# Kernel tuning notes

Hardware: AMD Instinct MI355X
Metric: run time of the kernel (lower is better)

Reference implementation:

```python
import jax, jax.numpy as jnp
from jax import lax
import numpy as np

T, B, H, NUM_DATA, IN_DIM = 2048, 256, 128, 4096, 1


def setup_inputs() -> dict:
    key = jax.random.key(0)
    ks = jax.random.split(key, 9)
    s = 1.0 / np.sqrt(H)  # PyTorch LSTM/Linear default init scale
    inp = {
        "input": jax.random.normal(ks[0], (T, B, IN_DIM), dtype=jnp.float32),
        "label": jax.random.randint(ks[1], (B,), 0, NUM_DATA),
        "h0": jnp.zeros((1, NUM_DATA, H), dtype=jnp.float32),
        "W_ih": jax.random.uniform(ks[2], (4 * H, IN_DIM), jnp.float32, -s, s),
        "W_hh": jax.random.uniform(ks[3], (4 * H, H), jnp.float32, -s, s),
        "b_ih": jax.random.uniform(ks[4], (4 * H,), jnp.float32, -s, s),
        "b_hh": jax.random.uniform(ks[5], (4 * H,), jnp.float32, -s, s),
        "W_lin": jax.random.uniform(ks[6], (IN_DIM, H), jnp.float32, -s, s),
        "b_lin": jax.random.uniform(ks[7], (IN_DIM,), jnp.float32, -s, s),
    }
    return inp


def reference(input, label, h0, W_ih, W_hh, b_ih, b_hh, W_lin, b_lin):
    seq_len = input.shape[0]
    num_in_batch = input.shape[1]
    # Gather learned initial hidden state per sequence id (the python cat loop in torch)
    h = h0[0, label]                                   # (B, H)
    c = jnp.zeros_like(h)                              # (B, H)
    y0 = jnp.zeros((num_in_batch, IN_DIM), input.dtype)  # t=0 input is zeros
    b = b_ih + b_hh                                    # (4H,)

    def step(carry, _):
        h, c, x = carry
        gates = x @ W_ih.T + h @ W_hh.T + b            # (B, 4H); torch gate order i,f,g,o
        i, f, g, o = jnp.split(gates, 4, axis=-1)
        i = jax.nn.sigmoid(i)
        f = jax.nn.sigmoid(f)
        g = jnp.tanh(g)
        o = jax.nn.sigmoid(o)
        c = f * c + i * g
        h = o * jnp.tanh(c)
        y = h @ W_lin.T + b_lin                        # (B, 1) -> fed back as next input
        return (h, c, y), y

    _, ys = lax.scan(step, (h, c, y0), None, length=seq_len)
    return ys  # (T, B, 1), matches torch cat of (1, B, 1) along dim 0
```

## Files before the change

### kernel.cpp

```cpp
#include <hip/hip_runtime.h>
#include <math.h>

#define T_STEPS 2048
#define BATCH   256
#define HDIM    128

__device__ __forceinline__ float fast_rcp(float x) { return __builtin_amdgcn_rcpf(x); }
__device__ __forceinline__ float sigmoid_f(float x) { return fast_rcp(1.0f + __expf(-x)); }
__device__ __forceinline__ float tanh_f(float x) {
    float e = __expf(2.0f * x);
    return 1.0f - 2.0f * fast_rcp(e + 1.0f);
}

#define REP8(M) M(0) M(1) M(2) M(3) M(4) M(5) M(6) M(7)

__global__ __launch_bounds__(512, 2)
void lstm_seq_kernel(const int*   __restrict__ label,
                     const float* __restrict__ h0,
                     const float* __restrict__ W_ih,
                     const float* __restrict__ W_hh,
                     const float* __restrict__ b_ih,
                     const float* __restrict__ b_hh,
                     const float* __restrict__ W_lin,
                     const float* __restrict__ b_lin,
                     float*       __restrict__ out)
{
    const int tid   = threadIdx.x;
    const int batch = blockIdx.x;
    const int m     = tid >> 2;
    const int q     = tid & 3;
    const int q8    = q * 8;

    const int ri = m, rf = m + 128, rg = m + 256, ro = m + 384;

    __shared__ __attribute__((aligned(16))) float hist[128 * 144];

    const float4* W4 = (const float4*)W_hh;
    const float4* L4 = (const float4*)W_lin;

    #define DECL_W(i) \
        float4 wi##i = W4[ri * 32 + q8 + (i)]; \
        float4 wf##i = W4[rf * 32 + q8 + (i)]; \
        float4 wg##i = W4[rg * 32 + q8 + (i)]; \
        float4 wo##i = W4[ro * 32 + q8 + (i)];
    REP8(DECL_W)

    const float wih_i = W_ih[ri], wih_f = W_ih[rf];
    const float wih_g = W_ih[rg], wih_o = W_ih[ro];
    const float blin  = b_lin[0];

    const float bi_ = b_ih[ri] + b_hh[ri] + wih_i * blin;
    const float bf_ = b_ih[rf] + b_hh[rf] + wih_f * blin;
    const float bg_ = b_ih[rg] + b_hh[rg] + wih_g * blin;
    const float bo_ = b_ih[ro] + b_hh[ro] + wih_o * blin;

    const float SNEG = -0x1.715476p+0f;
    const float SG   =  0x1.715476p+1f;
    const float bi4s = bi_ * 0.25f * SNEG;
    const float bf4s = bf_ * 0.25f * SNEG;
    const float bg4s = bg_ * 0.25f * SG;
    const float bo4s = bo_ * 0.25f * SNEG;

    #define FOLD_W(i) { float4 lv = L4[q8 + (i)]; \
        wi##i.x = fmaf(wih_i, lv.x, wi##i.x); wi##i.y = fmaf(wih_i, lv.y, wi##i.y); \
        wi##i.z = fmaf(wih_i, lv.z, wi##i.z); wi##i.w = fmaf(wih_i, lv.w, wi##i.w); \
        wf##i.x = fmaf(wih_f, lv.x, wf##i.x); wf##i.y = fmaf(wih_f, lv.y, wf##i.y); \
        wf##i.z = fmaf(wih_f, lv.z, wf##i.z); wf##i.w = fmaf(wih_f, lv.w, wf##i.w); \
        wg##i.x = fmaf(wih_g, lv.x, wg##i.x); wg##i.y = fmaf(wih_g, lv.y, wg##i.y); \
        wg##i.z = fmaf(wih_g, lv.z, wg##i.z); wg##i.w = fmaf(wih_g, lv.w, wg##i.w); \
        wo##i.x = fmaf(wih_o, lv.x, wo##i.x); wo##i.y = fmaf(wih_o, lv.y, wo##i.y); \
        wo##i.z = fmaf(wih_o, lv.z, wo##i.z); wo##i.w = fmaf(wih_o, lv.w, wo##i.w); }
    REP8(FOLD_W)

    const int   lane = tid & 63;
    const int   ya0w = lane + ((lane >> 5) << 2);
    const float wl_a = W_lin[lane];
    const float wl_b = W_lin[lane + 64];
    const int   hword = m + ((m >> 5) << 2);

    float* slotI = &hist[144 * 127];
    if (tid < HDIM) slotI[tid + ((tid >> 5) << 2)] = h0[label[batch] * HDIM + tid];
    __syncthreads();

    float p0 = slotI[ya0w] * wl_a + slotI[ya0w + 72] * wl_b;
    #pragma unroll
    for (int off = 1; off < 64; off <<= 1) p0 += __shfl_xor(p0, off, 64);
    const float y0 = p0 + blin;

    const float cbi = bi_ - wih_i * y0;
    const float cbf = bf_ - wih_f * y0;
    const float cbg = bg_ - wih_g * y0;
    const float cbo = bo_ - wih_o * y0;

    const float4* hq0 = (const float4*)(slotI + 36 * q);
    float ai = 0.f, af = 0.f, ag = 0.f, ao = 0.f;
    #define DOT4(i) { float4 hv = hq0[(i)]; \
        ai = fmaf(hv.x, wi##i.x, ai); ai = fmaf(hv.y, wi##i.y, ai); \
        ai = fmaf(hv.z, wi##i.z, ai); ai = fmaf(hv.w, wi##i.w, ai); \
        af = fmaf(hv.x, wf##i.x, af); af = fmaf(hv.y, wf##i.y, af); \
        af = fmaf(hv.z, wf##i.z, af); af = fmaf(hv.w, wf##i.w, af); \
        ag = fmaf(hv.x, wg##i.x, ag); ag = fmaf(hv.y, wg##i.y, ag); \
        ag = fmaf(hv.z, wg##i.z, ag); ag = fmaf(hv.w, wg##i.w, ag); \
        ao = fmaf(hv.x, wo##i.x, ao); ao = fmaf(hv.y, wo##i.y, ao); \
        ao = fmaf(hv.z, wo##i.z, ao); ao = fmaf(hv.w, wo##i.w, ao); }
    REP8(DOT4)
    ai += __shfl_xor(ai, 1, 64); af += __shfl_xor(af, 1, 64);
    ag += __shfl_xor(ag, 1, 64); ao += __shfl_xor(ao, 1, 64);
    ai += __shfl_xor(ai, 2, 64); af += __shfl_xor(af, 2, 64);
    ag += __shfl_xor(ag, 2, 64); ao += __shfl_xor(ao, 2, 64);
    const float iv0 = sigmoid_f(ai + cbi);
    const float fv0 = sigmoid_f(af + cbf);
    const float gv0 = tanh_f  (ag + cbg);
    const float ov0 = sigmoid_f(ao + cbo);
    float c = iv0 * gv0;
    const float hn0 = ov0 * tanh_f(c);
    if (q == 0) hist[hword] = hn0;
    __syncthreads();

    const unsigned histB = (unsigned)(unsigned long long)(&hist[0]);
    const unsigned vR0 = histB + 144u * (unsigned)q;
    const unsigned hW0 = histB + 576u + 4u * (unsigned)hword;
    const unsigned vD0 = (unsigned)(-576 + 144 * q - 4 * hword);
    const unsigned fR0 = histB + 576u * (unsigned)m + 144u * (unsigned)q;
    const unsigned jO0 = 1024u * (unsigned)m;
    const unsigned vO0 = 4u * (unsigned)batch;
    const unsigned offI = (unsigned)(ri * 512 + q * 128);
    const unsigned offF = (unsigned)(rf * 512 + q * 128);
    const unsigned offG = (unsigned)(rg * 512 + q * 128);
    const unsigned offO = (unsigned)(ro * 512 + q * 128);
    const unsigned offL = (unsigned)(q * 128);

    asm volatile(
        "v_mov_b32 v220, %[bi]\n\t"
        "v_mov_b32 v221, 0\n\t"
        "v_mov_b32 v222, %[bf]\n\t"
        "v_mov_b32 v223, 0\n\t"
        "v_mov_b32 v224, %[bg]\n\t"
        "v_mov_b32 v225, 0\n\t"
        "v_mov_b32 v226, %[bo]\n\t"
        "v_mov_b32 v227, 0\n\t"
        "v_mov_b32 v185, %[blin]\n\t"
        "v_mov_b32 v168, %[c0]\n\t"
        "v_mov_b32 v172, %[vR]\n\t"
        "v_mov_b32 v174, %[hW]\n\t"
        "v_mov_b32 v186, %[vD]\n\t"
        "v_mov_b32 v184, %[fR]\n\t"
        "v_mov_b32 v171, %[jO]\n\t"
        "v_mov_b32 v176, %[vO]\n\t"
        "v_and_b32 v170, 3, %[tid]\n\t"
        "v_cmp_eq_u32 vcc, 0, v170\n\t"
        "s_nop 4\n\t"
        "s_mov_b64 s[26:27], vcc\n\t"
        "global_load_dwordx4 v[32:35], %[offI], %[whh] offset:0\n\t"
        "global_load_dwordx4 v[36:39], %[offI], %[whh] offset:16\n\t"
        "global_load_dwordx4 v[40:43], %[offI], %[whh] offset:32\n\t"
        "global_load_dwordx4 v[44:47], %[offI], %[whh] offset:48\n\t"
        "global_load_dwordx4 v[48:51], %[offI], %[whh] offset:64\n\t"
        "global_load_dwordx4 v[52:55], %[offI], %[whh] offset:80\n\t"
        "global_load_dwordx4 v[56:59], %[offI], %[whh] offset:96\n\t"
        "global_load_dwordx4 v[60:63], %[offI], %[whh] offset:112\n\t"
        "global_load_dwordx4 v[64:67], %[offF], %[whh] offset:0\n\t"
        "global_load_dwordx4 v[68:71], %[offF], %[whh] offset:16\n\t"
        "global_load_dwordx4 v[72:75], %[offF], %[whh] offset:32\n\t"
        "global_load_dwordx4 v[76:79], %[offF], %[whh] offset:48\n\t"
        "global_load_dwordx4 v[80:83], %[offF], %[whh] offset:64\n\t"
        "global_load_dwordx4 v[84:87], %[offF], %[whh] offset:80\n\t"
        "global_load_dwordx4 v[88:91], %[offF], %[whh] offset:96\n\t"
        "global_load_dwordx4 v[92:95], %[offF], %[whh] offset:112\n\t"
        "global_load_dwordx4 v[96:99], %[offG], %[whh] offset:0\n\t"
        "global_load_dwordx4 v[100:103], %[offG], %[whh] offset:16\n\t"
        "global_load_dwordx4 v[104:107], %[offG], %[whh] offset:32\n\t"
        "global_load_dwordx4 v[108:111], %[offG], %[whh] offset:48\n\t"
        "global_load_dwordx4 v[112:115], %[offG], %[whh] offset:64\n\t"
        "global_load_dwordx4 v[116:119], %[offG], %[whh] offset:80\n\t"
        "global_load_dwordx4 v[120:123], %[offG], %[whh] offset:96\n\t"
        "global_load_dwordx4 v[124:127], %[offG], %[whh] offset:112\n\t"
        "global_load_dwordx4 v[128:131], %[offO], %[whh] offset:0\n\t"
        "global_load_dwordx4 v[132:135], %[offO], %[whh] offset:16\n\t"
        "global_load_dwordx4 v[136:139], %[offO], %[whh] offset:32\n\t"
        "global_load_dwordx4 v[140:143], %[offO], %[whh] offset:48\n\t"
        "global_load_dwordx4 v[144:147], %[offO], %[whh] offset:64\n\t"
        "global_load_dwordx4 v[148:151], %[offO], %[whh] offset:80\n\t"
        "global_load_dwordx4 v[152:155], %[offO], %[whh] offset:96\n\t"
        "global_load_dwordx4 v[156:159], %[offO], %[whh] offset:112\n\t"
        "global_load_dwordx4 v[188:191], %[offL], %[wlin] offset:0\n\t"
        "global_load_dwordx4 v[192:195], %[offL], %[wlin] offset:16\n\t"
        "global_load_dwordx4 v[196:199], %[offL], %[wlin] offset:32\n\t"
        "global_load_dwordx4 v[200:203], %[offL], %[wlin] offset:48\n\t"
        "global_load_dwordx4 v[204:207], %[offL], %[wlin] offset:64\n\t"
        "global_load_dwordx4 v[208:211], %[offL], %[wlin] offset:80\n\t"
        "global_load_dwordx4 v[212:215], %[offL], %[wlin] offset:96\n\t"
        "global_load_dwordx4 v[216:219], %[offL], %[wlin] offset:112\n\t"
        "s_waitcnt vmcnt(0)\n\t"
        ".set K_I, 0\n"
        ".rept 32\n"
        " v_fma_f32 v[32+K_I],  %[wihi], v[188+K_I], v[32+K_I]\n"
        " v_fma_f32 v[64+K_I],  %[wihf], v[188+K_I], v[64+K_I]\n"
        " v_fma_f32 v[96+K_I],  %[wihg], v[188+K_I], v[96+K_I]\n"
        " v_fma_f32 v[128+K_I], %[wiho], v[188+K_I], v[128+K_I]\n"
        " .set K_I, K_I+1\n"
        ".endr\n"
        ".set K_I, 0\n"
        ".rept 32\n"
        " v_mul_f32 v[32+K_I],  0xbfb8aa3b, v[32+K_I]\n"
        " v_mul_f32 v[64+K_I],  0xbfb8aa3b, v[64+K_I]\n"
        " v_mul_f32 v[96+K_I],  0x4038aa3b, v[96+K_I]\n"
        " v_mul_f32 v[128+K_I], 0xbfb8aa3b, v[128+K_I]\n"
        " .set K_I, K_I+1\n"
        ".endr\n"
        "s_movk_i32 s24, 1\n\t"
        "1:\n\t"
        "ds_read_b128 v[0:3],   v172\n\t"
        "ds_read_b128 v[4:7],   v172 offset:16\n\t"
        "ds_read_b128 v[8:11],  v172 offset:32\n\t"
        "ds_read_b128 v[12:15], v172 offset:48\n\t"
        "ds_read_b128 v[16:19], v172 offset:64\n\t"
        "ds_read_b128 v[20:23], v172 offset:80\n\t"
        "ds_read_b128 v[24:27], v172 offset:96\n\t"
        "ds_read_b128 v[28:31], v172 offset:112\n\t"
        "s_waitcnt lgkmcnt(6)\n\t"
        "v_pk_fma_f32 v[160:161], v[0:1], v[32:33], v[220:221]\n\t"
        "v_pk_fma_f32 v[162:163], v[0:1], v[64:65], v[222:223]\n\t"
        "v_pk_fma_f32 v[164:165], v[0:1], v[96:97], v[224:225]\n\t"
        "v_pk_fma_f32 v[166:167], v[0:1], v[128:129], v[226:227]\n\t"
        ".set K_I, 2\n"
        ".rept 3\n"
        " v_pk_fma_f32 v[160:161], v[K_I:K_I+1], v[32+K_I:33+K_I], v[160:161]\n"
        " v_pk_fma_f32 v[162:163], v[K_I:K_I+1], v[64+K_I:65+K_I], v[162:163]\n"
        " v_pk_fma_f32 v[164:165], v[K_I:K_I+1], v[96+K_I:97+K_I], v[164:165]\n"
        " v_pk_fma_f32 v[166:167], v[K_I:K_I+1], v[128+K_I:129+K_I], v[166:167]\n"
        " .set K_I, K_I+2\n"
        ".endr\n"
        "s_waitcnt lgkmcnt(4)\n\t"
        ".rept 4\n"
        " v_pk_fma_f32 v[160:161], v[K_I:K_I+1], v[32+K_I:33+K_I], v[160:161]\n"
        " v_pk_fma_f32 v[162:163], v[K_I:K_I+1], v[64+K_I:65+K_I], v[162:163]\n"
        " v_pk_fma_f32 v[164:165], v[K_I:K_I+1], v[96+K_I:97+K_I], v[164:165]\n"
        " v_pk_fma_f32 v[166:167], v[K_I:K_I+1], v[128+K_I:129+K_I], v[166:167]\n"
        " .set K_I, K_I+2\n"
        ".endr\n"
        "s_waitcnt lgkmcnt(2)\n\t"
        ".rept 4\n"
        " v_pk_fma_f32 v[160:161], v[K_I:K_I+1], v[32+K_I:33+K_I], v[160:161]\n"
        " v_pk_fma_f32 v[162:163], v[K_I:K_I+1], v[64+K_I:65+K_I], v[162:163]\n"
        " v_pk_fma_f32 v[164:165], v[K_I:K_I+1], v[96+K_I:97+K_I], v[164:165]\n"
        " v_pk_fma_f32 v[166:167], v[K_I:K_I+1], v[128+K_I:129+K_I], v[166:167]\n"
        " .set K_I, K_I+2\n"
        ".endr\n"
        "s_waitcnt lgkmcnt(0)\n\t"
        ".rept 4\n"
        " v_pk_fma_f32 v[160:161], v[K_I:K_I+1], v[32+K_I:33+K_I], v[160:161]\n"
        " v_pk_fma_f32 v[162:163], v[K_I:K_I+1], v[64+K_I:65+K_I], v[162:163]\n"
        " v_pk_fma_f32 v[164:165], v[K_I:K_I+1], v[96+K_I:97+K_I], v[164:165]\n"
        " v_pk_fma_f32 v[166:167], v[K_I:K_I+1], v[128+K_I:129+K_I], v[166:167]\n"
        " .set K_I, K_I+2\n"
        ".endr\n"
        "v_add_f32 v160, v160, v161\n\t"
        "v_add_f32 v161, v162, v163\n\t"
        "v_add_f32 v164, v164, v165\n\t"
        "v_add_f32 v165, v166, v167\n\t"
        "v_add_f32_dpp v160, v160, v160 quad_perm:[1,0,3,2] row_mask:0xf bank_mask:0xf\n\t"
        "v_add_f32_dpp v161, v161, v161 quad_perm:[1,0,3,2] row_mask:0xf bank_mask:0xf\n\t"
        "v_add_f32_dpp v164, v164, v164 quad_perm:[1,0,3,2] row_mask:0xf bank_mask:0xf\n\t"
        "v_add_f32_dpp v165, v165, v165 quad_perm:[1,0,3,2] row_mask:0xf bank_mask:0xf\n\t"
        "v_add_f32_dpp v160, v160, v160 quad_perm:[2,3,0,1] row_mask:0xf bank_mask:0xf\n\t"
        "v_add_f32_dpp v161, v161, v161 quad_perm:[2,3,0,1] row_mask:0xf bank_mask:0xf\n\t"
        "v_add_f32_dpp v164, v164, v164 quad_perm:[2,3,0,1] row_mask:0xf bank_mask:0xf\n\t"
        "v_add_f32_dpp v165, v165, v165 quad_perm:[2,3,0,1] row_mask:0xf bank_mask:0xf\n\t"
        "v_exp_f32 v160, v160\n\t"
        "v_exp_f32 v161, v161\n\t"
        "v_exp_f32 v164, v164\n\t"
        "v_exp_f32 v165, v165\n\t"
        "v_add_f32 v164, 1.0, v164\n\t"
        "v_add_f32 v165, 1.0, v165\n\t"
        "v_add_f32 v160, 1.0, v160\n\t"
        "v_add_f32 v161, 1.0, v161\n\t"
        "v_rcp_f32 v164, v164\n\t"
        "v_rcp_f32 v160, v160\n\t"
        "v_rcp_f32 v161, v161\n\t"
        "v_rcp_f32 v165, v165\n\t"
        "v_fma_f32 v164, -2.0, v164, 1.0\n\t"
        "v_mul_f32 v170, v160, v164\n\t"
        "v_fma_f32 v168, v161, v168, v170\n\t"
        "v_mul_f32 v170, 0x4038aa3b, v168\n\t"
        "v_exp_f32 v170, v170\n\t"
        "s_nop 1\n\t"
        "v_add_f32 v170, 1.0, v170\n\t"
        "v_rcp_f32 v170, v170\n\t"
        "s_nop 1\n\t"
        "v_fma_f32 v169, -2.0, v170, 1.0\n\t"
        "v_mul_f32 v169, v165, v169\n\t"
        "s_mov_b64 s[22:23], exec\n\t"
        "s_mov_b64 exec, s[26:27]\n\t"
        "ds_write_b32 v174, v169\n\t"
        "s_mov_b64 exec, s[22:23]\n\t"
        "v_add_u32 v174, 0x240, v174\n\t"
        "v_add_u32 v172, v174, v186\n\t"
        "s_waitcnt lgkmcnt(0)\n\t"
        "s_barrier\n\t"
        "s_and_b32 s20, s24, 127\n\t"
        "s_cmp_lg_u32 s20, 127\n\t"
        "s_cbranch_scc1 3f\n\t"
        "v_add_u32 v174, 0xfffee000, v174\n\t"
        "ds_read_b128 v[0:3],   v184\n\t"
        "ds_read_b128 v[4:7],   v184 offset:16\n\t"
        "ds_read_b128 v[8:11],  v184 offset:32\n\t"
        "ds_read_b128 v[12:15], v184 offset:48\n\t"
        "ds_read_b128 v[16:19], v184 offset:64\n\t"
        "ds_read_b128 v[20:23], v184 offset:80\n\t"
        "ds_read_b128 v[24:27], v184 offset:96\n\t"
        "ds_read_b128 v[28:31], v184 offset:112\n\t"
        "v_mov_b32 v164, 0\n\t"
        "s_waitcnt lgkmcnt(0)\n\t"
        ".set K_I, 0\n"
        ".rept 32\n"
        " v_fma_f32 v164, v[0+K_I], v[188+K_I], v164\n"
        " .set K_I, K_I+1\n"
        ".endr\n"
        "s_nop 1\n\t"
        "v_add_f32_dpp v164, v164, v164 quad_perm:[1,0,3,2] row_mask:0xf bank_mask:0xf\n\t"
        "s_nop 1\n\t"
        "v_add_f32_dpp v164, v164, v164 quad_perm:[2,3,0,1] row_mask:0xf bank_mask:0xf\n\t"
        "v_add_f32 v164, v164, v185\n\t"
        "v_add_u32 v170, v176, v171\n\t"
        "s_mov_b64 s[22:23], exec\n\t"
        "s_mov_b64 exec, s[26:27]\n\t"
        "global_store_dword v170, v164, %[outp]\n\t"
        "s_mov_b64 exec, s[22:23]\n\t"
        "v_add_u32 v176, 0x20000, v176\n\t"
        "s_barrier\n\t"
        "3:\n\t"
        "s_add_i32 s24, s24, 1\n\t"
        "s_cmp_lt_i32 s24, 2048\n\t"
        "s_cbranch_scc1 1b\n\t"
        :
        : [offI]"v"(offI), [offF]"v"(offF), [offG]"v"(offG), [offO]"v"(offO),
          [offL]"v"(offL), [whh]"s"(W_hh), [wlin]"s"(W_lin), [outp]"s"(out),
          [wihi]"v"(wih_i), [wihf]"v"(wih_f), [wihg]"v"(wih_g), [wiho]"v"(wih_o),
          [bi]"v"(bi4s), [bf]"v"(bf4s), [bg]"v"(bg4s), [bo]"v"(bo4s),
          [blin]"v"(blin), [c0]"v"(c),
          [vR]"v"(vR0), [hW]"v"(hW0), [vD]"v"(vD0), [fR]"v"(fR0),
          [jO]"v"(jO0), [vO]"v"(vO0), [tid]"v"(tid)
        : "memory", "scc", "vcc", "s20","s21","s22","s23","s24","s25","s26","s27",
          "v0","v1","v2","v3","v4","v5","v6","v7","v8","v9",
          "v10","v11","v12","v13","v14","v15","v16","v17","v18","v19",
          "v20","v21","v22","v23","v24","v25","v26","v27","v28","v29",
          "v30","v31","v32","v33","v34","v35","v36","v37","v38","v39",
          "v40","v41","v42","v43","v44","v45","v46","v47","v48","v49",
          "v50","v51","v52","v53","v54","v55","v56","v57","v58","v59",
          "v60","v61","v62","v63","v64","v65","v66","v67","v68","v69",
          "v70","v71","v72","v73","v74","v75","v76","v77","v78","v79",
          "v80","v81","v82","v83","v84","v85","v86","v87","v88","v89",
          "v90","v91","v92","v93","v94","v95","v96","v97","v98","v99",
          "v100","v101","v102","v103","v104","v105","v106","v107","v108","v109",
          "v110","v111","v112","v113","v114","v115","v116","v117","v118","v119",
          "v120","v121","v122","v123","v124","v125","v126","v127","v128","v129",
          "v130","v131","v132","v133","v134","v135","v136","v137","v138","v139",
          "v140","v141","v142","v143","v144","v145","v146","v147","v148","v149",
          "v150","v151","v152","v153","v154","v155","v156","v157","v158","v159",
          "v160","v161","v162","v163","v164","v165","v166","v167","v168","v169",
          "v170","v171","v172","v173","v174","v175","v176","v177","v178","v179",
          "v180","v181","v182","v183","v184","v185","v186","v187","v188","v189",
          "v190","v191","v192","v193","v194","v195","v196","v197","v198","v199",
          "v200","v201","v202","v203","v204","v205","v206","v207","v208","v209",
          "v210","v211","v212","v213","v214","v215","v216","v217","v218","v219",
          "v220","v221","v222","v223","v224","v225","v226","v227");
}

extern "C" void kernel_launch(void* const* d_in, const int* in_sizes, int n_in,
                              void* d_out, int out_size, void* d_ws, size_t ws_size,
                              hipStream_t stream) {
    const int*   label = (const int*)  d_in[1];
    const float* h0    = (const float*)d_in[2];
    const float* W_ih  = (const float*)d_in[3];
    const float* W_hh  = (const float*)d_in[4];
    const float* b_ih  = (const float*)d_in[5];
    const float* b_hh  = (const float*)d_in[6];
    const float* W_lin = (const float*)d_in[7];
    const float* b_lin = (const float*)d_in[8];
    float* out = (float*)d_out;

    lstm_seq_kernel<<<dim3(BATCH), dim3(512), 0, stream>>>(
        label, h0, W_ih, W_hh, b_ih, b_hh, W_lin, b_lin, out);
}
```

Before: 1.179 ms.

## Distribute gate activations across quad lanes via permuted weight rows

Each lane in a 4-lane quad now holds the gate weights in an XOR-permuted order, so after a single combined DPP reduction every lane owns a different gate's pre-activation. Each lane evaluates one exp/rcp activation instead of all four, and the results are exchanged with DPP moves before the cell update. This shortens the serial transcendental chain on the per-step critical path. The cost is extra DPP traffic and s_nop hazard padding, plus per-lane scale and bias selection. The history write mask becomes a constant lane pattern and the write pointer updates move earlier in the step.

```diff
diff --git a/kernel.cpp b/kernel.cpp
--- a/kernel.cpp
+++ b/kernel.cpp
@@ -56,10 +56,25 @@
 
     const float SNEG = -0x1.715476p+0f;
     const float SG   =  0x1.715476p+1f;
-    const float bi4s = bi_ * 0.25f * SNEG;
-    const float bf4s = bf_ * 0.25f * SNEG;
-    const float bg4s = bg_ * 0.25f * SG;
-    const float bo4s = bo_ * 0.25f * SNEG;
+    const float sI = bi_ * 0.25f * SNEG;
+    const float sF = bf_ * 0.25f * SNEG;
+    const float sG_ = bg_ * 0.25f * SG;
+    const float sO = bo_ * 0.25f * SNEG;
+
+    const float b0s = (q==0)?sI :(q==1)?sF :(q==2)?sG_:sO;
+    const float b1s = (q==0)?sF :(q==1)?sI :(q==2)?sO :sG_;
+    const float b2s = (q==0)?sG_:(q==1)?sO :(q==2)?sI :sF;
+    const float b3s = (q==0)?sO :(q==1)?sG_:(q==2)?sF :sI;
+    const float wihA = (q==0)?wih_i:(q==1)?wih_f:(q==2)?wih_g:wih_o;
+    const float wihB = (q==0)?wih_f:(q==1)?wih_i:(q==2)?wih_o:wih_g;
+    const float wihC = (q==0)?wih_g:(q==1)?wih_o:(q==2)?wih_i:wih_f;
+    const float wihD = (q==0)?wih_o:(q==1)?wih_g:(q==2)?wih_f:wih_i;
+    const float sc0 = ( q     == 2) ? SG : SNEG;
+    const float sc1 = ((q^1)  == 2) ? SG : SNEG;
+    const float sc2 = ((q^2)  == 2) ? SG : SNEG;
+    const float sc3 = ((q^3)  == 2) ? SG : SNEG;
+    const float caq = (q==2) ? -2.0f : 1.0f;
+    const float cbq = (q==2) ?  1.0f : 0.0f;
 
     #define FOLD_W(i) { float4 lv = L4[q8 + (i)]; \
         wi##i.x = fmaf(wih_i, lv.x, wi##i.x); wi##i.y = fmaf(wih_i, lv.y, wi##i.y); \
@@ -119,25 +134,25 @@
 
     const unsigned histB = (unsigned)(unsigned long long)(&hist[0]);
     const unsigned vR0 = histB + 144u * (unsigned)q;
-    const unsigned hW0 = histB + 576u + 4u * (unsigned)hword;
-    const unsigned vD0 = (unsigned)(-576 + 144 * q - 4 * hword);
+    const unsigned hW0 = histB + 4u * (unsigned)hword;
+    const unsigned vD0 = (unsigned)(144 * q - 4 * hword);
     const unsigned fR0 = histB + 576u * (unsigned)m + 144u * (unsigned)q;
     const unsigned jO0 = 1024u * (unsigned)m;
     const unsigned vO0 = 4u * (unsigned)batch;
-    const unsigned offI = (unsigned)(ri * 512 + q * 128);
-    const unsigned offF = (unsigned)(rf * 512 + q * 128);
-    const unsigned offG = (unsigned)(rg * 512 + q * 128);
-    const unsigned offO = (unsigned)(ro * 512 + q * 128);
+    const unsigned off0 = (unsigned)((m + 128 * (q    )) * 512 + q * 128);
+    const unsigned off1 = (unsigned)((m + 128 * (q ^ 1)) * 512 + q * 128);
+    const unsigned off2 = (unsigned)((m + 128 * (q ^ 2)) * 512 + q * 128);
+    const unsigned off3 = (unsigned)((m + 128 * (q ^ 3)) * 512 + q * 128);
     const unsigned offL = (unsigned)(q * 128);
 
     asm volatile(
-        "v_mov_b32 v220, %[bi]\n\t"
+        "v_mov_b32 v220, %[b0]\n\t"
         "v_mov_b32 v221, 0\n\t"
-        "v_mov_b32 v222, %[bf]\n\t"
+        "v_mov_b32 v222, %[b1]\n\t"
         "v_mov_b32 v223, 0\n\t"
-        "v_mov_b32 v224, %[bg]\n\t"
+        "v_mov_b32 v224, %[b2]\n\t"
         "v_mov_b32 v225, 0\n\t"
-        "v_mov_b32 v226, %[bo]\n\t"
+        "v_mov_b32 v226, %[b3]\n\t"
         "v_mov_b32 v227, 0\n\t"
         "v_mov_b32 v185, %[blin]\n\t"
         "v_mov_b32 v168, %[c0]\n\t"
@@ -147,42 +162,40 @@
         "v_mov_b32 v184, %[fR]\n\t"
         "v_mov_b32 v171, %[jO]\n\t"
         "v_mov_b32 v176, %[vO]\n\t"
-        "v_and_b32 v170, 3, %[tid]\n\t"
-        "v_cmp_eq_u32 vcc, 0, v170\n\t"
-        "s_nop 4\n\t"
-        "s_mov_b64 s[26:27], vcc\n\t"
-        "global_load_dwordx4 v[32:35], %[offI], %[whh] offset:0\n\t"
-        "global_load_dwordx4 v[36:39], %[offI], %[whh] offset:16\n\t"
-        "global_load_dwordx4 v[40:43], %[offI], %[whh] offset:32\n\t"
-        "global_load_dwordx4 v[44:47], %[offI], %[whh] offset:48\n\t"
-        "global_load_dwordx4 v[48:51], %[offI], %[whh] offset:64\n\t"
-        "global_load_dwordx4 v[52:55], %[offI], %[whh] offset:80\n\t"
-        "global_load_dwordx4 v[56:59], %[offI], %[whh] offset:96\n\t"
-        "global_load_dwordx4 v[60:63], %[offI], %[whh] offset:112\n\t"
-        "global_load_dwordx4 v[64:67], %[offF], %[whh] offset:0\n\t"
-        "global_load_dwordx4 v[68:71], %[offF], %[whh] offset:16\n\t"
-        "global_load_dwordx4 v[72:75], %[offF], %[whh] offset:32\n\t"
-        "global_load_dwordx4 v[76:79], %[offF], %[whh] offset:48\n\t"
-        "global_load_dwordx4 v[80:83], %[offF], %[whh] offset:64\n\t"
-        "global_load_dwordx4 v[84:87], %[offF], %[whh] offset:80\n\t"
-        "global_load_dwordx4 v[88:91], %[offF], %[whh] offset:96\n\t"
-        "global_load_dwordx4 v[92:95], %[offF], %[whh] offset:112\n\t"
-        "global_load_dwordx4 v[96:99], %[offG], %[whh] offset:0\n\t"
-        "global_load_dwordx4 v[100:103], %[offG], %[whh] offset:16\n\t"
-        "global_load_dwordx4 v[104:107], %[offG], %[whh] offset:32\n\t"
-        "global_load_dwordx4 v[108:111], %[offG], %[whh] offset:48\n\t"
-        "global_load_dwordx4 v[112:115], %[offG], %[whh] offset:64\n\t"
-        "global_load_dwordx4 v[116:119], %[offG], %[whh] offset:80\n\t"
-        "global_load_dwordx4 v[120:123], %[offG], %[whh] offset:96\n\t"
-        "global_load_dwordx4 v[124:127], %[offG], %[whh] offset:112\n\t"
-        "global_load_dwordx4 v[128:131], %[offO], %[whh] offset:0\n\t"
-        "global_load_dwordx4 v[132:135], %[offO], %[whh] offset:16\n\t"
-        "global_load_dwordx4 v[136:139], %[offO], %[whh] offset:32\n\t"
-        "global_load_dwordx4 v[140:143], %[offO], %[whh] offset:48\n\t"
-        "global_load_dwordx4 v[144:147], %[offO], %[whh] offset:64\n\t"
-        "global_load_dwordx4 v[148:151], %[offO], %[whh] offset:80\n\t"
-        "global_load_dwordx4 v[152:155], %[offO], %[whh] offset:96\n\t"
-        "global_load_dwordx4 v[156:159], %[offO], %[whh] offset:112\n\t"
+        "s_mov_b32 s26, 0x11111111\n\t"
+        "s_mov_b32 s27, 0x11111111\n\t"
+        "global_load_dwordx4 v[32:35], %[off0], %[whh] offset:0\n\t"
+        "global_load_dwordx4 v[36:39], %[off0], %[whh] offset:16\n\t"
+        "global_load_dwordx4 v[40:43], %[off0], %[whh] offset:32\n\t"
+        "global_load_dwordx4 v[44:47], %[off0], %[whh] offset:48\n\t"
+        "global_load_dwordx4 v[48:51], %[off0], %[whh] offset:64\n\t"
+        "global_load_dwordx4 v[52:55], %[off0], %[whh] offset:80\n\t"
+        "global_load_dwordx4 v[56:59], %[off0], %[whh] offset:96\n\t"
+        "global_load_dwordx4 v[60:63], %[off0], %[whh] offset:112\n\t"
+        "global_load_dwordx4 v[64:67], %[off1], %[whh] offset:0\n\t"
+        "global_load_dwordx4 v[68:71], %[off1], %[whh] offset:16\n\t"
+        "global_load_dwordx4 v[72:75], %[off1], %[whh] offset:32\n\t"
+        "global_load_dwordx4 v[76:79], %[off1], %[whh] offset:48\n\t"
+        "global_load_dwordx4 v[80:83], %[off1], %[whh] offset:64\n\t"
+        "global_load_dwordx4 v[84:87], %[off1], %[whh] offset:80\n\t"
+        "global_load_dwordx4 v[88:91], %[off1], %[whh] offset:96\n\t"
+        "global_load_dwordx4 v[92:95], %[off1], %[whh] offset:112\n\t"
+        "global_load_dwordx4 v[96:99], %[off2], %[whh] offset:0\n\t"
+        "global_load_dwordx4 v[100:103], %[off2], %[whh] offset:16\n\t"
+        "global_load_dwordx4 v[104:107], %[off2], %[whh] offset:32\n\t"
+        "global_load_dwordx4 v[108:111], %[off2], %[whh] offset:48\n\t"
+        "global_load_dwordx4 v[112:115], %[off2], %[whh] offset:64\n\t"
+        "global_load_dwordx4 v[116:119], %[off2], %[whh] offset:80\n\t"
+        "global_load_dwordx4 v[120:123], %[off2], %[whh] offset:96\n\t"
+        "global_load_dwordx4 v[124:127], %[off2], %[whh] offset:112\n\t"
+        "global_load_dwordx4 v[128:131], %[off3], %[whh] offset:0\n\t"
+        "global_load_dwordx4 v[132:135], %[off3], %[whh] offset:16\n\t"
+        "global_load_dwordx4 v[136:139], %[off3], %[whh] offset:32\n\t"
+        "global_load_dwordx4 v[140:143], %[off3], %[whh] offset:48\n\t"
+        "global_load_dwordx4 v[144:147], %[off3], %[whh] offset:64\n\t"
+        "global_load_dwordx4 v[148:151], %[off3], %[whh] offset:80\n\t"
+        "global_load_dwordx4 v[152:155], %[off3], %[whh] offset:96\n\t"
+        "global_load_dwordx4 v[156:159], %[off3], %[whh] offset:112\n\t"
         "global_load_dwordx4 v[188:191], %[offL], %[wlin] offset:0\n\t"
         "global_load_dwordx4 v[192:195], %[offL], %[wlin] offset:16\n\t"
         "global_load_dwordx4 v[196:199], %[offL], %[wlin] offset:32\n\t"
@@ -194,18 +207,18 @@
         "s_waitcnt vmcnt(0)\n\t"
         ".set K_I, 0\n"
         ".rept 32\n"
-        " v_fma_f32 v[32+K_I],  %[wihi], v[188+K_I], v[32+K_I]\n"
-        " v_fma_f32 v[64+K_I],  %[wihf], v[188+K_I], v[64+K_I]\n"
-        " v_fma_f32 v[96+K_I],  %[wihg], v[188+K_I], v[96+K_I]\n"
-        " v_fma_f32 v[128+K_I], %[wiho], v[188+K_I], v[128+K_I]\n"
+        " v_fma_f32 v[32+K_I],  %[wA], v[188+K_I], v[32+K_I]\n"
+        " v_fma_f32 v[64+K_I],  %[wB], v[188+K_I], v[64+K_I]\n"
+        " v_fma_f32 v[96+K_I],  %[wC], v[188+K_I], v[96+K_I]\n"
+        " v_fma_f32 v[128+K_I], %[wD], v[188+K_I], v[128+K_I]\n"
         " .set K_I, K_I+1\n"
         ".endr\n"
         ".set K_I, 0\n"
         ".rept 32\n"
-        " v_mul_f32 v[32+K_I],  0xbfb8aa3b, v[32+K_I]\n"
-        " v_mul_f32 v[64+K_I],  0xbfb8aa3b, v[64+K_I]\n"
-        " v_mul_f32 v[96+K_I],  0x4038aa3b, v[96+K_I]\n"
-        " v_mul_f32 v[128+K_I], 0xbfb8aa3b, v[128+K_I]\n"
+        " v_mul_f32 v[32+K_I],  %[sc0], v[32+K_I]\n"
+        " v_mul_f32 v[64+K_I],  %[sc1], v[64+K_I]\n"
+        " v_mul_f32 v[96+K_I],  %[sc2], v[96+K_I]\n"
+        " v_mul_f32 v[128+K_I], %[sc3], v[128+K_I]\n"
         " .set K_I, K_I+1\n"
         ".endr\n"
         "s_movk_i32 s24, 1\n\t"
@@ -259,43 +272,38 @@
         "v_add_f32 v161, v162, v163\n\t"
         "v_add_f32 v164, v164, v165\n\t"
         "v_add_f32 v165, v166, v167\n\t"
-        "v_add_f32_dpp v160, v160, v160 quad_perm:[1,0,3,2] row_mask:0xf bank_mask:0xf\n\t"
-        "v_add_f32_dpp v161, v161, v161 quad_perm:[1,0,3,2] row_mask:0xf bank_mask:0xf\n\t"
-        "v_add_f32_dpp v164, v164, v164 quad_perm:[1,0,3,2] row_mask:0xf bank_mask:0xf\n\t"
-        "v_add_f32_dpp v165, v165, v165 quad_perm:[1,0,3,2] row_mask:0xf bank_mask:0xf\n\t"
-        "v_add_f32_dpp v160, v160, v160 quad_perm:[2,3,0,1] row_mask:0xf bank_mask:0xf\n\t"
-        "v_add_f32_dpp v161, v161, v161 quad_perm:[2,3,0,1] row_mask:0xf bank_mask:0xf\n\t"
-        "v_add_f32_dpp v164, v164, v164 quad_perm:[2,3,0,1] row_mask:0xf bank_mask:0xf\n\t"
-        "v_add_f32_dpp v165, v165, v165 quad_perm:[2,3,0,1] row_mask:0xf bank_mask:0xf\n\t"
+        "s_nop 1\n\t"
+        "v_add_f32_dpp v160, v161, v160 quad_perm:[1,0,3,2] row_mask:0xf bank_mask:0xf\n\t"
+        "v_add_f32_dpp v164, v165, v164 quad_perm:[1,0,3,2] row_mask:0xf bank_mask:0xf\n\t"
+        "v_add_u32 v174, 0x240, v174\n\t"
+        "v_add_u32 v172, v174, v186\n\t"
+        "s_nop 1\n\t"
+        "v_add_f32_dpp v160, v164, v160 quad_perm:[2,3,0,1] row_mask:0xf bank_mask:0xf\n\t"
+        "s_nop 3\n\t"
         "v_exp_f32 v160, v160\n\t"
-        "v_exp_f32 v161, v161\n\t"
-        "v_exp_f32 v164, v164\n\t"
-        "v_exp_f32 v165, v165\n\t"
-        "v_add_f32 v164, 1.0, v164\n\t"
-        "v_add_f32 v165, 1.0, v165\n\t"
+        "s_nop 1\n\t"
         "v_add_f32 v160, 1.0, v160\n\t"
-        "v_add_f32 v161, 1.0, v161\n\t"
-        "v_rcp_f32 v164, v164\n\t"
         "v_rcp_f32 v160, v160\n\t"
-        "v_rcp_f32 v161, v161\n\t"
-        "v_rcp_f32 v165, v165\n\t"
-        "v_fma_f32 v164, -2.0, v164, 1.0\n\t"
-        "v_mul_f32 v170, v160, v164\n\t"
-        "v_fma_f32 v168, v161, v168, v170\n\t"
-        "v_mul_f32 v170, 0x4038aa3b, v168\n\t"
-        "v_exp_f32 v170, v170\n\t"
-        "s_nop 1\n\t"
-        "v_add_f32 v170, 1.0, v170\n\t"
-        "v_rcp_f32 v170, v170\n\t"
-        "s_nop 1\n\t"
-        "v_fma_f32 v169, -2.0, v170, 1.0\n\t"
-        "v_mul_f32 v169, v165, v169\n\t"
+        "s_nop 1\n\t"
+        "v_fma_f32 v166, %[ca], v160, %[cb]\n\t"
+        "s_nop 3\n\t"
+        "v_mul_f32_dpp v161, v166, v166 quad_perm:[2,3,0,1] row_mask:0xf bank_mask:0xf\n\t"
+        "v_mov_b32_dpp v162, v166 quad_perm:[1,0,3,2] row_mask:0xf bank_mask:0xf\n\t"
+        "v_mov_b32_dpp v165, v166 quad_perm:[3,3,3,3] row_mask:0xf bank_mask:0xf\n\t"
+        "s_nop 2\n\t"
+        "v_fma_f32 v168, v162, v168, v161\n\t"
+        "v_mul_f32 v163, 0x4038aa3b, v168\n\t"
+        "v_exp_f32 v163, v163\n\t"
+        "s_nop 1\n\t"
+        "v_add_f32 v163, 1.0, v163\n\t"
+        "v_rcp_f32 v163, v163\n\t"
+        "s_nop 1\n\t"
+        "v_fma_f32 v163, -2.0, v163, 1.0\n\t"
+        "v_mul_f32 v169, v165, v163\n\t"
         "s_mov_b64 s[22:23], exec\n\t"
         "s_mov_b64 exec, s[26:27]\n\t"
         "ds_write_b32 v174, v169\n\t"
         "s_mov_b64 exec, s[22:23]\n\t"
-        "v_add_u32 v174, 0x240, v174\n\t"
-        "v_add_u32 v172, v174, v186\n\t"
         "s_waitcnt lgkmcnt(0)\n\t"
         "s_barrier\n\t"
         "s_and_b32 s20, s24, 127\n\t"
@@ -334,13 +342,15 @@
         "s_cmp_lt_i32 s24, 2048\n\t"
         "s_cbranch_scc1 1b\n\t"
         :
-        : [offI]"v"(offI), [offF]"v"(offF), [offG]"v"(offG), [offO]"v"(offO),
+        : [off0]"v"(off0), [off1]"v"(off1), [off2]"v"(off2), [off3]"v"(off3),
           [offL]"v"(offL), [whh]"s"(W_hh), [wlin]"s"(W_lin), [outp]"s"(out),
-          [wihi]"v"(wih_i), [wihf]"v"(wih_f), [wihg]"v"(wih_g), [wiho]"v"(wih_o),
-          [bi]"v"(bi4s), [bf]"v"(bf4s), [bg]"v"(bg4s), [bo]"v"(bo4s),
-          [blin]"v"(blin), [c0]"v"(c),
+          [wA]"v"(wihA), [wB]"v"(wihB), [wC]"v"(wihC), [wD]"v"(wihD),
+          [b0]"v"(b0s), [b1]"v"(b1s), [b2]"v"(b2s), [b3]"v"(b3s),
+          [sc0]"v"(sc0), [sc1]"v"(sc1), [sc2]"v"(sc2), [sc3]"v"(sc3),
+          [ca]"v"(caq), [cb]"v"(cbq),
+          [blin]"s"(blin), [c0]"v"(c),
           [vR]"v"(vR0), [hW]"v"(hW0), [vD]"v"(vD0), [fR]"v"(fR0),
-          [jO]"v"(jO0), [vO]"v"(vO0), [tid]"v"(tid)
+          [jO]"v"(jO0), [vO]"s"(vO0)
         : "memory", "scc", "vcc", "s20","s21","s22","s23","s24","s25","s26","s27",
           "v0","v1","v2","v3","v4","v5","v6","v7","v8","v9",
           "v10","v11","v12","v13","v14","v15","v16","v17","v18","v19",
```

New measurement: 1.126 ms, median of 2. 1.05x faster.
